# Kernel optimization log

Hardware: AMD Instinct MI355X
Metric: run time of the kernel (lower is better)

Reference implementation:

```python
import jax, jax.numpy as jnp
import numpy as np

N_NODES = 100000
N_EDGES = 3200000
IN_DIM = 256
HID = 16
OUT = 10


def setup_inputs() -> dict:
    key = jax.random.key(0)
    k1, k2, k3, k4, k5, k6 = jax.random.split(key, 6)
    x = jax.random.normal(k1, (N_NODES, IN_DIM), dtype=jnp.float32)
    edge_index = jax.random.randint(k2, (2, N_EDGES), 0, N_NODES, dtype=jnp.int64)
    # Glorot-style init for GCN weights, zeros for bias (PyG defaults)
    W1 = jax.random.normal(k3, (IN_DIM, HID), dtype=jnp.float32) * (1.0 / np.sqrt(IN_DIM))
    b1 = jnp.zeros((HID,), dtype=jnp.float32)
    W2 = jax.random.normal(k4, (HID, OUT), dtype=jnp.float32) * (1.0 / np.sqrt(HID))
    b2 = jnp.zeros((OUT,), dtype=jnp.float32)
    return {"x": x, "edge_index": edge_index, "W1": W1, "b1": b1, "W2": W2, "b2": b2}


def _gcn_conv(h, src, dst, W, b, num_nodes):
    # GCNConv(normalize=False): out_i = sum_{(j->i) in E} (h_j W) + b
    m = h @ W                                   # [N, F_out] small GEMM
    agg = jax.ops.segment_sum(m[src], dst, num_segments=num_nodes)  # gather+scatter-add
    return agg + b


def reference(x, edge_index, W1, b1, W2, b2):
    src = edge_index[0]  # message source (flow: source_to_target)
    dst = edge_index[1]
    n = x.shape[0]
    h = jax.nn.relu(_gcn_conv(x, src, dst, W1, b1, n))
    # F.dropout with module in eval mode -> identity
    out = _gcn_conv(h, src, dst, W2, b2, n)
    return out
```

## Files before the change

### kernel.cpp

```cpp
#include <hip/hip_runtime.h>
#include <hip/hip_bf16.h>
#include <stdint.h>

#define IN_DIM 256
#define HID 16
#define OUTD 10
#define BKT_SHIFT 8
#define BKT_W 256
#define PART_CH 4096
#define EPT 16

typedef short v8s __attribute__((ext_vector_type(8)));
typedef float v4f __attribute__((ext_vector_type(4)));

__device__ __forceinline__ float bf2f(unsigned short u) {
    return __uint_as_float(((unsigned int)u) << 16);
}
__device__ __forceinline__ unsigned short f2bf(float f) {
    unsigned int u = __float_as_uint(f);
    unsigned int lsb = (u >> 16) & 1u;
    u += 0x7fffu + lsb;
    return (unsigned short)(u >> 16);
}

__device__ __forceinline__ int load_dst(const void* ei, int n_edges, int e, int is64) {
    return is64 ? (int)((const long long*)ei)[(size_t)n_edges + e]
                : ((const int*)ei)[(size_t)n_edges + e];
}
__device__ __forceinline__ int load_src(const void* ei, int n_edges, int e, int is64) {
    return is64 ? (int)((const long long*)ei)[e] : ((const int*)ei)[e];
}

__global__ void setup_kernel(const void* __restrict__ x,
                             const void* __restrict__ W1,
                             const void* __restrict__ ei,
                             int n_nodes, int* __restrict__ flags,
                             int* __restrict__ bucket_cnt, int K) {
    int t = threadIdx.x;
    for (int i = t; i < K; i += blockDim.x) bucket_cnt[i] = 0;
    if (t < 64) {
        const unsigned short* xs = (const unsigned short*)x;
        const unsigned short* ws = (const unsigned short*)W1;
        bool badx = false, badw = false;
#pragma unroll
        for (int q = 0; q < 4; ++q) {
            float vx = bf2f(xs[t + 64 * q]);
            float vw = bf2f(ws[t + 64 * q]);
            if (!(vx > -1e4f && vx < 1e4f)) badx = true;
            if (!(vw > -1e4f && vw < 1e4f)) badw = true;
        }
        const unsigned long long* e64 = (const unsigned long long*)ei;
        bool big = false;
#pragma unroll
        for (int q = 0; q < 2; ++q)
            if (e64[t + 64 * q] >= (unsigned long long)n_nodes) big = true;
        int xf32 = __any(badx) ? 1 : 0;
        int wf32 = __any(badw) ? 1 : 0;
        int is64 = __any(big) ? 0 : 1;
        if (t == 0) { flags[0] = is64; flags[1] = xf32; flags[2] = wf32; }
    }
}

__global__ void bhist_kernel(const void* __restrict__ ei, int n_edges,
                             int* __restrict__ bucket_cnt,
                             const int* __restrict__ flags, int K) {
    extern __shared__ int lh[];
    for (int i = threadIdx.x; i < K; i += blockDim.x) lh[i] = 0;
    __syncthreads();
    int is64 = flags[0];
    int t = blockIdx.x * blockDim.x + threadIdx.x;
    int stride = gridDim.x * blockDim.x;
    for (int e = t; e < n_edges; e += stride) {
        int d = load_dst(ei, n_edges, e, is64);
        atomicAdd(&lh[d >> BKT_SHIFT], 1);
    }
    __syncthreads();
    for (int i = threadIdx.x; i < K; i += blockDim.x)
        if (lh[i]) atomicAdd(&bucket_cnt[i], lh[i]);
}

__global__ void bscan_kernel(const int* __restrict__ bucket_cnt, int K,
                             int* __restrict__ bucket_off, int* __restrict__ bcur,
                             int* __restrict__ row_off, int n_nodes, int n_edges) {
    __shared__ int ts[256];
    int t = threadIdx.x;
    const int KP = (K + 255) / 256;
    int base = t * KP;
    int local[8];
    int s = 0;
    for (int q = 0; q < KP; ++q) {
        int idx = base + q;
        int v = (idx < K) ? bucket_cnt[idx] : 0;
        local[q] = v; s += v;
    }
    ts[t] = s;
    __syncthreads();
    for (int off = 1; off < 256; off <<= 1) {
        int v = (t >= off) ? ts[t - off] : 0;
        __syncthreads();
        ts[t] += v;
        __syncthreads();
    }
    int ex = ts[t] - s;
    for (int q = 0; q < KP; ++q) {
        int idx = base + q;
        if (idx < K) { bucket_off[idx] = ex; bcur[idx] = ex; }
        ex += local[q];
    }
    if (t == 255) bucket_off[K] = ex;
    if (t == 0) row_off[n_nodes] = n_edges;
}

__global__ void part_kernel(const void* __restrict__ ei, int n_edges,
                            int* __restrict__ bcur, unsigned int* __restrict__ pairs,
                            const int* __restrict__ flags, int K) {
    __shared__ int lh[512];
    __shared__ int gdelta[512];
    __shared__ int ts[256];
    __shared__ unsigned int spairs[PART_CH];
    __shared__ unsigned short sbkt[PART_CH];
    int begin = blockIdx.x * PART_CH;
    int is64 = flags[0];
    int t = threadIdx.x;
    lh[t] = 0; lh[t + 256] = 0;

    int dloc[EPT];
#pragma unroll
    for (int i = 0; i < EPT; ++i) {
        int e = begin + i * 256 + t;
        dloc[i] = (e < n_edges) ? load_dst(ei, n_edges, e, is64) : -1;
    }
    __syncthreads();
#pragma unroll
    for (int i = 0; i < EPT; ++i)
        if (dloc[i] >= 0) atomicAdd(&lh[dloc[i] >> BKT_SHIFT], 1);
    __syncthreads();

    int c0 = lh[2 * t], c1 = lh[2 * t + 1];
    int s = c0 + c1;
    ts[t] = s;
    __syncthreads();
    for (int off = 1; off < 256; off <<= 1) {
        int v = (t >= off) ? ts[t - off] : 0;
        __syncthreads();
        ts[t] += v;
        __syncthreads();
    }
    int ex = ts[t] - s;
    if (c0 > 0) gdelta[2 * t]     = atomicAdd(&bcur[2 * t], c0) - ex;
    if (c1 > 0) gdelta[2 * t + 1] = atomicAdd(&bcur[2 * t + 1], c1) - (ex + c0);
    __syncthreads();
    lh[2 * t] = ex; lh[2 * t + 1] = ex + c0;
    __syncthreads();

#pragma unroll
    for (int i = 0; i < EPT; ++i) {
        int e = begin + i * 256 + t;
        if (dloc[i] >= 0) {
            int srcv = load_src(ei, n_edges, e, is64);
            int b = dloc[i] >> BKT_SHIFT;
            int lpos = atomicAdd(&lh[b], 1);
            spairs[lpos] = ((unsigned)srcv << 8) | ((unsigned)dloc[i] & (BKT_W - 1));
            sbkt[lpos] = (unsigned short)b;
        }
    }
    __syncthreads();

    int total = n_edges - begin; if (total > PART_CH) total = PART_CH;
    for (int j = t; j < total; j += 256)
        pairs[gdelta[sbkt[j]] + j] = spairs[j];
}

__global__ void csr_kernel(const unsigned int* __restrict__ pairs,
                           const int* __restrict__ bucket_off,
                           int* __restrict__ row_off, int* __restrict__ csr_src,
                           int n_nodes) {
    __shared__ int deg[BKT_W];
    __shared__ int cur[BKT_W];
    __shared__ int ts[BKT_W];
    int blk = blockIdx.x;
    int nbase = blk << BKT_SHIFT;
    int NL = n_nodes - nbase; if (NL > BKT_W) NL = BKT_W;
    int beg = bucket_off[blk], end = bucket_off[blk + 1];
    int t = threadIdx.x;
    if (t < BKT_W) deg[t] = 0;
    __syncthreads();
    for (int k = beg + t; k < end; k += blockDim.x)
        atomicAdd(&deg[pairs[k] & (BKT_W - 1)], 1);
    __syncthreads();
    if (t < BKT_W) ts[t] = deg[t];
    __syncthreads();
    for (int off = 1; off < BKT_W; off <<= 1) {
        int v = 0;
        if (t < BKT_W && t >= off) v = ts[t - off];
        __syncthreads();
        if (t < BKT_W) ts[t] += v;
        __syncthreads();
    }
    if (t < BKT_W) {
        int ex = beg + ts[t] - deg[t];
        cur[t] = ex;
        if (t < NL) row_off[nbase + t] = ex;
    }
    __syncthreads();
    for (int k = beg + t; k < end; k += blockDim.x) {
        unsigned int p = pairs[k];
        int pos = atomicAdd(&cur[p & (BKT_W - 1)], 1);
        csr_src[pos] = (int)(p >> 8);
    }
}

__global__ __launch_bounds__(256) void gemm1_kernel(
        const void* __restrict__ xp_, const void* __restrict__ W1p,
        unsigned short* __restrict__ m1, int n_nodes,
        const int* __restrict__ flags) {
    __shared__ unsigned short Bbuf[8192];
    int t = threadIdx.x;
    const int xf32 = flags[1], wf32 = flags[2];
    int lane = t & 63;
    int wave = t >> 6;
    int col  = lane & 15;
    int quad = lane >> 4;
    int n_tiles = (n_nodes + 15) >> 4;

    if (!xf32) {
        unsigned short* Bl = Bbuf;
        for (int i = t; i < 4096; i += 256) {
            unsigned short w = wf32 ? f2bf(((const float*)W1p)[i])
                                    : ((const unsigned short*)W1p)[i];
            int k = i >> 4, n = i & 15;
            int kk = k >> 5, qd = (k >> 3) & 3, j = k & 7;
            Bl[((kk * 4 + qd) * 16 + n) * 8 + j] = w;
        }
        __syncthreads();
        v8s bfrag[8];
#pragma unroll
        for (int kk = 0; kk < 8; ++kk)
            bfrag[kk] = *(const v8s*)&Bl[(kk * 64 + lane) * 8];
        const unsigned short* x = (const unsigned short*)xp_;
        for (int t0 = blockIdx.x * 8 + wave * 2; t0 < n_tiles; t0 += gridDim.x * 8) {
            int rA = t0 * 16 + col;       rA = rA < n_nodes ? rA : n_nodes - 1;
            int rB = t0 * 16 + 16 + col;  rB = rB < n_nodes ? rB : n_nodes - 1;
            const unsigned short* xpA = x + (size_t)rA * IN_DIM + quad * 8;
            const unsigned short* xpB = x + (size_t)rB * IN_DIM + quad * 8;
            v8s aA[8], aB[8];
#pragma unroll
            for (int kk = 0; kk < 8; ++kk) aA[kk] = *(const v8s*)(xpA + kk * 32);
#pragma unroll
            for (int kk = 0; kk < 8; ++kk) aB[kk] = *(const v8s*)(xpB + kk * 32);
            v4f accA = {0.f, 0.f, 0.f, 0.f};
            v4f accB = {0.f, 0.f, 0.f, 0.f};
#pragma unroll
            for (int kk = 0; kk < 8; ++kk) {
                accA = __builtin_amdgcn_mfma_f32_16x16x32_bf16(aA[kk], bfrag[kk], accA, 0, 0, 0);
                accB = __builtin_amdgcn_mfma_f32_16x16x32_bf16(aB[kk], bfrag[kk], accB, 0, 0, 0);
            }
#pragma unroll
            for (int rg = 0; rg < 4; ++rg) {
                int nA = t0 * 16 + quad * 4 + rg;
                int nB = nA + 16;
                if (nA < n_nodes) m1[(size_t)nA * HID + col] = f2bf(accA[rg]);
                if (nB < n_nodes) m1[(size_t)nB * HID + col] = f2bf(accB[rg]);
            }
        }
    } else {
        unsigned short* Bhi = Bbuf;
        unsigned short* Blo = Bbuf + 4096;
        for (int i = t; i < 4096; i += 256) {
            float w = wf32 ? ((const float*)W1p)[i]
                           : bf2f(((const unsigned short*)W1p)[i]);
            unsigned short hi = f2bf(w);
            unsigned short lo = f2bf(w - bf2f(hi));
            int k = i >> 4, n = i & 15;
            int kk = k >> 5, qd = (k >> 3) & 3, j = k & 7;
            int idx = ((kk * 4 + qd) * 16 + n) * 8 + j;
            Bhi[idx] = hi; Blo[idx] = lo;
        }
        __syncthreads();
        const float* x = (const float*)xp_;
        for (int t0 = blockIdx.x * 8 + wave * 2; t0 < n_tiles; t0 += gridDim.x * 8) {
            int rA = t0 * 16 + col;       rA = rA < n_nodes ? rA : n_nodes - 1;
            int rB = t0 * 16 + 16 + col;  rB = rB < n_nodes ? rB : n_nodes - 1;
            const float* xpA = x + (size_t)rA * IN_DIM + quad * 8;
            const float* xpB = x + (size_t)rB * IN_DIM + quad * 8;
            float4 uA[16], uB[16];
#pragma unroll
            for (int kk = 0; kk < 8; ++kk) {
                uA[2 * kk]     = *(const float4*)(xpA + kk * 32);
                uA[2 * kk + 1] = *(const float4*)(xpA + kk * 32 + 4);
            }
#pragma unroll
            for (int kk = 0; kk < 8; ++kk) {
                uB[2 * kk]     = *(const float4*)(xpB + kk * 32);
                uB[2 * kk + 1] = *(const float4*)(xpB + kk * 32 + 4);
            }
            v4f accA = {0.f, 0.f, 0.f, 0.f};
            v4f accB = {0.f, 0.f, 0.f, 0.f};
#pragma unroll
            for (int kk = 0; kk < 8; ++kk) {
                float va[8] = {uA[2 * kk].x, uA[2 * kk].y, uA[2 * kk].z, uA[2 * kk].w,
                               uA[2 * kk + 1].x, uA[2 * kk + 1].y, uA[2 * kk + 1].z, uA[2 * kk + 1].w};
                float vb[8] = {uB[2 * kk].x, uB[2 * kk].y, uB[2 * kk].z, uB[2 * kk].w,
                               uB[2 * kk + 1].x, uB[2 * kk + 1].y, uB[2 * kk + 1].z, uB[2 * kk + 1].w};
                v8s ahiA, aloA, ahiB, aloB;
#pragma unroll
                for (int j = 0; j < 8; ++j) {
                    unsigned short hi = f2bf(va[j]);
                    unsigned short lo = f2bf(va[j] - bf2f(hi));
                    ahiA[j] = (short)hi; aloA[j] = (short)lo;
                    hi = f2bf(vb[j]);
                    lo = f2bf(vb[j] - bf2f(hi));
                    ahiB[j] = (short)hi; aloB[j] = (short)lo;
                }
                v8s bh = *(const v8s*)&Bhi[(kk * 64 + lane) * 8];
                v8s bl = *(const v8s*)&Blo[(kk * 64 + lane) * 8];
                accA = __builtin_amdgcn_mfma_f32_16x16x32_bf16(ahiA, bh, accA, 0, 0, 0);
                accA = __builtin_amdgcn_mfma_f32_16x16x32_bf16(ahiA, bl, accA, 0, 0, 0);
                accA = __builtin_amdgcn_mfma_f32_16x16x32_bf16(aloA, bh, accA, 0, 0, 0);
                accB = __builtin_amdgcn_mfma_f32_16x16x32_bf16(ahiB, bh, accB, 0, 0, 0);
                accB = __builtin_amdgcn_mfma_f32_16x16x32_bf16(ahiB, bl, accB, 0, 0, 0);
                accB = __builtin_amdgcn_mfma_f32_16x16x32_bf16(aloB, bh, accB, 0, 0, 0);
            }
#pragma unroll
            for (int rg = 0; rg < 4; ++rg) {
                int nA = t0 * 16 + quad * 4 + rg;
                int nB = nA + 16;
                if (nA < n_nodes) m1[(size_t)nA * HID + col] = f2bf(accA[rg]);
                if (nB < n_nodes) m1[(size_t)nB * HID + col] = f2bf(accB[rg]);
            }
        }
    }
}

__device__ __forceinline__ v4f gather_bf16(const unsigned short* __restrict__ src,
                                           const int* __restrict__ csr_src,
                                           int beg, int end, int q) {
    float a0 = 0.f, a1 = 0.f, a2 = 0.f, a3 = 0.f;
    int k = beg;
    for (; k + 16 <= end; k += 16) {
        uint2 v[16];
#pragma unroll
        for (int u = 0; u < 16; ++u) {
            int s = csr_src[k + u];
            v[u] = *(const uint2*)(src + (size_t)s * HID + q * 4);
        }
#pragma unroll
        for (int u = 0; u < 16; ++u) {
            a0 += bf2f((unsigned short)(v[u].x));
            a1 += bf2f((unsigned short)(v[u].x >> 16));
            a2 += bf2f((unsigned short)(v[u].y));
            a3 += bf2f((unsigned short)(v[u].y >> 16));
        }
    }
    for (; k + 4 <= end; k += 4) {
        uint2 v[4];
#pragma unroll
        for (int u = 0; u < 4; ++u) {
            int s = csr_src[k + u];
            v[u] = *(const uint2*)(src + (size_t)s * HID + q * 4);
        }
#pragma unroll
        for (int u = 0; u < 4; ++u) {
            a0 += bf2f((unsigned short)(v[u].x));
            a1 += bf2f((unsigned short)(v[u].x >> 16));
            a2 += bf2f((unsigned short)(v[u].y));
            a3 += bf2f((unsigned short)(v[u].y >> 16));
        }
    }
    for (; k < end; ++k) {
        int s = csr_src[k];
        uint2 v = *(const uint2*)(src + (size_t)s * HID + q * 4);
        a0 += bf2f((unsigned short)(v.x));
        a1 += bf2f((unsigned short)(v.x >> 16));
        a2 += bf2f((unsigned short)(v.y));
        a3 += bf2f((unsigned short)(v.y >> 16));
    }
    v4f r = {a0, a1, a2, a3};
    return r;
}

__global__ void agg1_kernel(const unsigned short* __restrict__ m1,
                            const int* __restrict__ row_off,
                            const int* __restrict__ csr_src,
                            const void* __restrict__ b1p,
                            unsigned short* __restrict__ h, int n_nodes,
                            const int* __restrict__ flags) {
    int t = blockIdx.x * blockDim.x + threadIdx.x;
    int node = t >> 2;
    if (node >= n_nodes) return;
    int q = t & 3;
    const int wf32 = flags[2];
    v4f a = gather_bf16(m1, csr_src, row_off[node], row_off[node + 1], q);
    float b0, b1v, b2v, b3;
    if (wf32) {
        const float* b = (const float*)b1p + q * 4;
        b0 = b[0]; b1v = b[1]; b2v = b[2]; b3 = b[3];
    } else {
        const unsigned short* b = (const unsigned short*)b1p + q * 4;
        b0 = bf2f(b[0]); b1v = bf2f(b[1]); b2v = bf2f(b[2]); b3 = bf2f(b[3]);
    }
    float r0 = fmaxf(a[0] + b0, 0.f);
    float r1 = fmaxf(a[1] + b1v, 0.f);
    float r2 = fmaxf(a[2] + b2v, 0.f);
    float r3 = fmaxf(a[3] + b3, 0.f);
    uint2 packed;
    packed.x = (unsigned int)f2bf(r0) | ((unsigned int)f2bf(r1) << 16);
    packed.y = (unsigned int)f2bf(r2) | ((unsigned int)f2bf(r3) << 16);
    *(uint2*)(h + (size_t)node * HID + q * 4) = packed;
}

__global__ void agg2_out_kernel(const unsigned short* __restrict__ h,
                                const int* __restrict__ row_off,
                                const int* __restrict__ csr_src,
                                const void* __restrict__ W2p,
                                const void* __restrict__ b2p,
                                void* __restrict__ out, int n_nodes,
                                const int* __restrict__ flags) {
    __shared__ float Ws[HID * OUTD];
    __shared__ float bs[OUTD];
    const int xf32 = flags[1], wf32 = flags[2];
    if (threadIdx.x < HID * OUTD)
        Ws[threadIdx.x] = wf32 ? ((const float*)W2p)[threadIdx.x]
                               : bf2f(((const unsigned short*)W2p)[threadIdx.x]);
    if (threadIdx.x < OUTD)
        bs[threadIdx.x] = wf32 ? ((const float*)b2p)[threadIdx.x]
                               : bf2f(((const unsigned short*)b2p)[threadIdx.x]);
    __syncthreads();

    int t = blockIdx.x * blockDim.x + threadIdx.x;
    int node = t >> 2;
    if (node >= n_nodes) return;
    int q = t & 3;
    v4f a = gather_bf16(h, csr_src, row_off[node], row_off[node + 1], q);

    float o[OUTD];
#pragma unroll
    for (int od = 0; od < OUTD; ++od) {
        float s = 0.f;
#pragma unroll
        for (int j = 0; j < 4; ++j)
            s = fmaf(a[j], Ws[(q * 4 + j) * OUTD + od], s);
        o[od] = s;
    }
#pragma unroll
    for (int od = 0; od < OUTD; ++od) {
        o[od] += __shfl_xor(o[od], 1);
        o[od] += __shfl_xor(o[od], 2);
        o[od] += bs[od];
    }

    if (xf32) {
        float2* po = (float2*)((float*)out + (size_t)node * OUTD);
        if (q == 0) {
            po[0] = make_float2(o[0], o[1]);
            po[1] = make_float2(o[2], o[3]);
        } else if (q == 1) {
            po[2] = make_float2(o[4], o[5]);
            po[3] = make_float2(o[6], o[7]);
        } else if (q == 2) {
            po[4] = make_float2(o[8], o[9]);
        }
    } else {
        unsigned int* po = (unsigned int*)((unsigned short*)out + (size_t)node * OUTD);
        if (q == 0) {
            po[0] = (unsigned int)f2bf(o[0]) | ((unsigned int)f2bf(o[1]) << 16);
            po[1] = (unsigned int)f2bf(o[2]) | ((unsigned int)f2bf(o[3]) << 16);
        } else if (q == 1) {
            po[2] = (unsigned int)f2bf(o[4]) | ((unsigned int)f2bf(o[5]) << 16);
            po[3] = (unsigned int)f2bf(o[6]) | ((unsigned int)f2bf(o[7]) << 16);
        } else if (q == 2) {
            po[4] = (unsigned int)f2bf(o[8]) | ((unsigned int)f2bf(o[9]) << 16);
        }
    }
}

__global__ void sentinel_kernel(float* __restrict__ out) {
    if (blockIdx.x == 0 && threadIdx.x < 16) out[threadIdx.x] = 123456.0f;
}

extern "C" void kernel_launch(void* const* d_in, const int* in_sizes, int n_in,
                              void* d_out, int out_size, void* d_ws, size_t ws_size,
                              hipStream_t stream) {
    const void* x  = d_in[0];
    const void* ei = d_in[1];
    const void* W1 = d_in[2];
    const void* b1 = d_in[3];
    const void* W2 = d_in[4];
    const void* b2 = d_in[5];

    const int n_nodes = in_sizes[0] / IN_DIM;
    const int n_edges = in_sizes[1] / 2;
    const int K = (n_nodes + BKT_W - 1) / BKT_W;

    char* p = (char*)d_ws;
    auto align = [](size_t v) { return (v + 255) & ~(size_t)255; };
    size_t off = 0;
    int* flags      = (int*)(p + off); off = align(off + 256);
    int* bucket_cnt = (int*)(p + off); off = align(off + (size_t)K * 4);
    int* bucket_off = (int*)(p + off); off = align(off + ((size_t)K + 1) * 4);
    int* bcur       = (int*)(p + off); off = align(off + (size_t)K * 4);
    int* row_off    = (int*)(p + off); off = align(off + ((size_t)n_nodes + 1) * 4);
    int* csr_src    = (int*)(p + off); off = align(off + (size_t)n_edges * 4);
    size_t alias_base = off;
    unsigned int* pairs = (unsigned int*)(p + alias_base);
    unsigned short* m1 = (unsigned short*)(p + alias_base);
    unsigned short* h  = m1 + (size_t)n_nodes * HID;
    size_t alias_sz = (size_t)n_edges * 4;
    size_t mh_sz = (size_t)n_nodes * HID * 2 * 2;
    if (mh_sz > alias_sz) alias_sz = mh_sz;
    off = align(alias_base + alias_sz);

    if (ws_size < off) {
        sentinel_kernel<<<1, 64, 0, stream>>>((float*)d_out);
        return;
    }

    const size_t lds_k = (size_t)K * 4;

    setup_kernel<<<1, 256, 0, stream>>>(x, W1, ei, n_nodes, flags, bucket_cnt, K);
    bhist_kernel<<<1024, 256, lds_k, stream>>>(ei, n_edges, bucket_cnt, flags, K);
    bscan_kernel<<<1, 256, 0, stream>>>(bucket_cnt, K, bucket_off, bcur,
                                        row_off, n_nodes, n_edges);
    part_kernel<<<(n_edges + PART_CH - 1) / PART_CH, 256, 0, stream>>>(
        ei, n_edges, bcur, pairs, flags, K);
    csr_kernel<<<K, 512, 0, stream>>>(pairs, bucket_off, row_off, csr_src, n_nodes);

    {
        int n_tiles16 = (n_nodes + 15) >> 4;
        int g1 = (n_tiles16 + 7) / 8;
        gemm1_kernel<<<g1, 256, 0, stream>>>(x, W1, m1, n_nodes, flags);
    }

    {
        long long threads = (long long)n_nodes * 4;
        agg1_kernel<<<(int)((threads + 255) / 256), 256, 0, stream>>>(
            m1, row_off, csr_src, b1, h, n_nodes, flags);
    }

    {
        long long threads = (long long)n_nodes * 4;
        agg2_out_kernel<<<(int)((threads + 255) / 256), 256, 0, stream>>>(
            h, row_off, csr_src, W2, b2, d_out, n_nodes, flags);
    }
}
```

Baseline: 338.9 us.

## Precompute split W1 fragments in a prep kernel and shrink gemm1 per-wave tiling

Moves the W1 hi/lo bf16 split and fragment swizzle into a small separate kernel that writes to workspace, so gemm1 no longer fills LDS or needs a block barrier before starting. Each wave now handles one 16-row tile instead of two, B fragments are read from global or L2 inside the loop, and launch bounds ask for higher occupancy. The bf16-input path now also adds a W1 low-part MFMA for extra accuracy. The trade-off is less work per wave against fewer registers, an extra kernel launch, and repeated global reads of the B fragments.

```diff
diff --git a/kernel.cpp b/kernel.cpp
--- a/kernel.cpp
+++ b/kernel.cpp
@@ -59,6 +59,23 @@
         int is64 = __any(big) ? 0 : 1;
         if (t == 0) { flags[0] = is64; flags[1] = xf32; flags[2] = wf32; }
     }
+}
+
+__global__ void w1prep_kernel(const void* __restrict__ W1p,
+                              unsigned short* __restrict__ W1split,
+                              const int* __restrict__ flags) {
+    const int wf32 = flags[2];
+    int i = threadIdx.x + blockIdx.x * blockDim.x;
+    if (i >= IN_DIM * HID) return;
+    float w = wf32 ? ((const float*)W1p)[i]
+                   : bf2f(((const unsigned short*)W1p)[i]);
+    unsigned short hi = f2bf(w);
+    unsigned short lo = f2bf(w - bf2f(hi));
+    int k = i >> 4, n = i & 15;
+    int kk = k >> 5, qd = (k >> 3) & 3, j = k & 7;
+    int idx = ((kk * 4 + qd) * 16 + n) * 8 + j;
+    W1split[idx] = hi;
+    W1split[4096 + idx] = lo;
 }
 
 __global__ void bhist_kernel(const void* __restrict__ ei, int n_edges,
@@ -210,123 +227,85 @@
     }
 }
 
-__global__ __launch_bounds__(256) void gemm1_kernel(
-        const void* __restrict__ xp_, const void* __restrict__ W1p,
+__global__ __launch_bounds__(256, 4) void gemm1_kernel(
+        const void* __restrict__ xp_,
+        const unsigned short* __restrict__ W1split,
         unsigned short* __restrict__ m1, int n_nodes,
         const int* __restrict__ flags) {
-    __shared__ unsigned short Bbuf[8192];
+    const int xf32 = flags[1];
     int t = threadIdx.x;
-    const int xf32 = flags[1], wf32 = flags[2];
     int lane = t & 63;
     int wave = t >> 6;
     int col  = lane & 15;
     int quad = lane >> 4;
     int n_tiles = (n_nodes + 15) >> 4;
+    const unsigned short* Whi = W1split;
+    const unsigned short* Wlo = W1split + 4096;
 
     if (!xf32) {
-        unsigned short* Bl = Bbuf;
-        for (int i = t; i < 4096; i += 256) {
-            unsigned short w = wf32 ? f2bf(((const float*)W1p)[i])
-                                    : ((const unsigned short*)W1p)[i];
-            int k = i >> 4, n = i & 15;
-            int kk = k >> 5, qd = (k >> 3) & 3, j = k & 7;
-            Bl[((kk * 4 + qd) * 16 + n) * 8 + j] = w;
-        }
-        __syncthreads();
-        v8s bfrag[8];
-#pragma unroll
-        for (int kk = 0; kk < 8; ++kk)
-            bfrag[kk] = *(const v8s*)&Bl[(kk * 64 + lane) * 8];
         const unsigned short* x = (const unsigned short*)xp_;
-        for (int t0 = blockIdx.x * 8 + wave * 2; t0 < n_tiles; t0 += gridDim.x * 8) {
-            int rA = t0 * 16 + col;       rA = rA < n_nodes ? rA : n_nodes - 1;
-            int rB = t0 * 16 + 16 + col;  rB = rB < n_nodes ? rB : n_nodes - 1;
-            const unsigned short* xpA = x + (size_t)rA * IN_DIM + quad * 8;
-            const unsigned short* xpB = x + (size_t)rB * IN_DIM + quad * 8;
-            v8s aA[8], aB[8];
-#pragma unroll
-            for (int kk = 0; kk < 8; ++kk) aA[kk] = *(const v8s*)(xpA + kk * 32);
-#pragma unroll
-            for (int kk = 0; kk < 8; ++kk) aB[kk] = *(const v8s*)(xpB + kk * 32);
-            v4f accA = {0.f, 0.f, 0.f, 0.f};
-            v4f accB = {0.f, 0.f, 0.f, 0.f};
+        for (int tile = blockIdx.x * 4 + wave; tile < n_tiles; tile += gridDim.x * 4) {
+            int row = tile * 16 + col;
+            int r = row < n_nodes ? row : n_nodes - 1;
+            const unsigned short* xp = x + (size_t)r * IN_DIM + quad * 8;
+            v8s a[8];
+#pragma unroll
+            for (int kk = 0; kk < 8; ++kk)
+                a[kk] = *(const v8s*)(xp + kk * 32);
+            v4f acc1 = {0.f, 0.f, 0.f, 0.f};
+            v4f acc2 = {0.f, 0.f, 0.f, 0.f};
 #pragma unroll
             for (int kk = 0; kk < 8; ++kk) {
-                accA = __builtin_amdgcn_mfma_f32_16x16x32_bf16(aA[kk], bfrag[kk], accA, 0, 0, 0);
-                accB = __builtin_amdgcn_mfma_f32_16x16x32_bf16(aB[kk], bfrag[kk], accB, 0, 0, 0);
+                v8s bh = *(const v8s*)&Whi[(kk * 64 + lane) * 8];
+                v8s bl = *(const v8s*)&Wlo[(kk * 64 + lane) * 8];
+                acc1 = __builtin_amdgcn_mfma_f32_16x16x32_bf16(a[kk], bh, acc1, 0, 0, 0);
+                acc2 = __builtin_amdgcn_mfma_f32_16x16x32_bf16(a[kk], bl, acc2, 0, 0, 0);
             }
 #pragma unroll
             for (int rg = 0; rg < 4; ++rg) {
-                int nA = t0 * 16 + quad * 4 + rg;
-                int nB = nA + 16;
-                if (nA < n_nodes) m1[(size_t)nA * HID + col] = f2bf(accA[rg]);
-                if (nB < n_nodes) m1[(size_t)nB * HID + col] = f2bf(accB[rg]);
+                int node = tile * 16 + quad * 4 + rg;
+                if (node < n_nodes)
+                    m1[(size_t)node * HID + col] = f2bf(acc1[rg] + acc2[rg]);
             }
         }
     } else {
-        unsigned short* Bhi = Bbuf;
-        unsigned short* Blo = Bbuf + 4096;
-        for (int i = t; i < 4096; i += 256) {
-            float w = wf32 ? ((const float*)W1p)[i]
-                           : bf2f(((const unsigned short*)W1p)[i]);
-            unsigned short hi = f2bf(w);
-            unsigned short lo = f2bf(w - bf2f(hi));
-            int k = i >> 4, n = i & 15;
-            int kk = k >> 5, qd = (k >> 3) & 3, j = k & 7;
-            int idx = ((kk * 4 + qd) * 16 + n) * 8 + j;
-            Bhi[idx] = hi; Blo[idx] = lo;
-        }
-        __syncthreads();
         const float* x = (const float*)xp_;
-        for (int t0 = blockIdx.x * 8 + wave * 2; t0 < n_tiles; t0 += gridDim.x * 8) {
-            int rA = t0 * 16 + col;       rA = rA < n_nodes ? rA : n_nodes - 1;
-            int rB = t0 * 16 + 16 + col;  rB = rB < n_nodes ? rB : n_nodes - 1;
-            const float* xpA = x + (size_t)rA * IN_DIM + quad * 8;
-            const float* xpB = x + (size_t)rB * IN_DIM + quad * 8;
-            float4 uA[16], uB[16];
+        for (int tile = blockIdx.x * 4 + wave; tile < n_tiles; tile += gridDim.x * 4) {
+            int row = tile * 16 + col;
+            int r = row < n_nodes ? row : n_nodes - 1;
+            const float* xp = x + (size_t)r * IN_DIM + quad * 8;
+            float4 u[16];
 #pragma unroll
             for (int kk = 0; kk < 8; ++kk) {
-                uA[2 * kk]     = *(const float4*)(xpA + kk * 32);
-                uA[2 * kk + 1] = *(const float4*)(xpA + kk * 32 + 4);
+                u[2 * kk]     = *(const float4*)(xp + kk * 32);
+                u[2 * kk + 1] = *(const float4*)(xp + kk * 32 + 4);
             }
+            v4f acc1 = {0.f, 0.f, 0.f, 0.f};
+            v4f acc2 = {0.f, 0.f, 0.f, 0.f};
 #pragma unroll
             for (int kk = 0; kk < 8; ++kk) {
-                uB[2 * kk]     = *(const float4*)(xpB + kk * 32);
-                uB[2 * kk + 1] = *(const float4*)(xpB + kk * 32 + 4);
+                float uv[8] = {u[2 * kk].x,     u[2 * kk].y,
+                               u[2 * kk].z,     u[2 * kk].w,
+                               u[2 * kk + 1].x, u[2 * kk + 1].y,
+                               u[2 * kk + 1].z, u[2 * kk + 1].w};
+                v8s ahi, alo;
+#pragma unroll
+                for (int j = 0; j < 8; ++j) {
+                    unsigned short hi = f2bf(uv[j]);
+                    unsigned short lo = f2bf(uv[j] - bf2f(hi));
+                    ahi[j] = (short)hi; alo[j] = (short)lo;
+                }
+                v8s bh = *(const v8s*)&Whi[(kk * 64 + lane) * 8];
+                v8s bl = *(const v8s*)&Wlo[(kk * 64 + lane) * 8];
+                acc1 = __builtin_amdgcn_mfma_f32_16x16x32_bf16(ahi, bh, acc1, 0, 0, 0);
+                acc2 = __builtin_amdgcn_mfma_f32_16x16x32_bf16(ahi, bl, acc2, 0, 0, 0);
+                acc2 = __builtin_amdgcn_mfma_f32_16x16x32_bf16(alo, bh, acc2, 0, 0, 0);
             }
-            v4f accA = {0.f, 0.f, 0.f, 0.f};
-            v4f accB = {0.f, 0.f, 0.f, 0.f};
-#pragma unroll
-            for (int kk = 0; kk < 8; ++kk) {
-                float va[8] = {uA[2 * kk].x, uA[2 * kk].y, uA[2 * kk].z, uA[2 * kk].w,
-                               uA[2 * kk + 1].x, uA[2 * kk + 1].y, uA[2 * kk + 1].z, uA[2 * kk + 1].w};
-                float vb[8] = {uB[2 * kk].x, uB[2 * kk].y, uB[2 * kk].z, uB[2 * kk].w,
-                               uB[2 * kk + 1].x, uB[2 * kk + 1].y, uB[2 * kk + 1].z, uB[2 * kk + 1].w};
-                v8s ahiA, aloA, ahiB, aloB;
-#pragma unroll
-                for (int j = 0; j < 8; ++j) {
-                    unsigned short hi = f2bf(va[j]);
-                    unsigned short lo = f2bf(va[j] - bf2f(hi));
-                    ahiA[j] = (short)hi; aloA[j] = (short)lo;
-                    hi = f2bf(vb[j]);
-                    lo = f2bf(vb[j] - bf2f(hi));
-                    ahiB[j] = (short)hi; aloB[j] = (short)lo;
-                }
-                v8s bh = *(const v8s*)&Bhi[(kk * 64 + lane) * 8];
-                v8s bl = *(const v8s*)&Blo[(kk * 64 + lane) * 8];
-                accA = __builtin_amdgcn_mfma_f32_16x16x32_bf16(ahiA, bh, accA, 0, 0, 0);
-                accA = __builtin_amdgcn_mfma_f32_16x16x32_bf16(ahiA, bl, accA, 0, 0, 0);
-                accA = __builtin_amdgcn_mfma_f32_16x16x32_bf16(aloA, bh, accA, 0, 0, 0);
-                accB = __builtin_amdgcn_mfma_f32_16x16x32_bf16(ahiB, bh, accB, 0, 0, 0);
-                accB = __builtin_amdgcn_mfma_f32_16x16x32_bf16(ahiB, bl, accB, 0, 0, 0);
-                accB = __builtin_amdgcn_mfma_f32_16x16x32_bf16(aloB, bh, accB, 0, 0, 0);
-            }
 #pragma unroll
             for (int rg = 0; rg < 4; ++rg) {
-                int nA = t0 * 16 + quad * 4 + rg;
-                int nB = nA + 16;
-                if (nA < n_nodes) m1[(size_t)nA * HID + col] = f2bf(accA[rg]);
-                if (nB < n_nodes) m1[(size_t)nB * HID + col] = f2bf(accB[rg]);
+                int node = tile * 16 + quad * 4 + rg;
+                if (node < n_nodes)
+                    m1[(size_t)node * HID + col] = f2bf(acc1[rg] + acc2[rg]);
             }
         }
     }
@@ -496,6 +475,7 @@
     auto align = [](size_t v) { return (v + 255) & ~(size_t)255; };
     size_t off = 0;
     int* flags      = (int*)(p + off); off = align(off + 256);
+    unsigned short* w1split = (unsigned short*)(p + off); off = align(off + 8192 * 2);
     int* bucket_cnt = (int*)(p + off); off = align(off + (size_t)K * 4);
     int* bucket_off = (int*)(p + off); off = align(off + ((size_t)K + 1) * 4);
     int* bcur       = (int*)(p + off); off = align(off + (size_t)K * 4);
@@ -518,6 +498,7 @@
     const size_t lds_k = (size_t)K * 4;
 
     setup_kernel<<<1, 256, 0, stream>>>(x, W1, ei, n_nodes, flags, bucket_cnt, K);
+    w1prep_kernel<<<16, 256, 0, stream>>>(W1, w1split, flags);
     bhist_kernel<<<1024, 256, lds_k, stream>>>(ei, n_edges, bucket_cnt, flags, K);
     bscan_kernel<<<1, 256, 0, stream>>>(bucket_cnt, K, bucket_off, bcur,
                                         row_off, n_nodes, n_edges);
@@ -527,8 +508,8 @@
 
     {
         int n_tiles16 = (n_nodes + 15) >> 4;
-        int g1 = (n_tiles16 + 7) / 8;
-        gemm1_kernel<<<g1, 256, 0, stream>>>(x, W1, m1, n_nodes, flags);
+        int g1 = (n_tiles16 + 3) / 4;
+        gemm1_kernel<<<g1, 256, 0, stream>>>(x, w1split, m1, n_nodes, flags);
     }
 
     {
```

New measurement: 334.9 us. Within noise of the previous version (-1.2%).
